# Performance work log

Measured on AMD Instinct MI355X. Metric: run time of the kernel, lower is better.

The kernel has to match this reference:

```python
import math
import jax, jax.numpy as jnp
import numpy as np

B, S, D = 1, 2048, 2048
H, KV, HD = 32, 4, 64  # n_heads, n_kv_heads, head_dim
N_REP = H // KV
ROPE_THETA = 10000.0


def setup_inputs() -> dict:
    key = jax.random.key(0)
    ks = jax.random.split(key, 6)
    x = jax.random.normal(ks[0], (B, S, D), dtype=jnp.float32)
    # precomputed rotary frequencies (real/imag parts of freqs_cis)
    inv_freq = 1.0 / (ROPE_THETA ** (jnp.arange(0, HD, 2, dtype=jnp.float32) / HD))  # [HD/2]
    t = jnp.arange(S, dtype=jnp.float32)
    ang = jnp.outer(t, inv_freq)  # [S, HD/2]
    freqs_cos = jnp.cos(ang)
    freqs_sin = jnp.sin(ang)
    # additive causal mask (large negative instead of -inf; numerically equivalent)
    mask = jnp.where(jnp.tril(jnp.ones((S, S), dtype=bool)), 0.0, -1e9).astype(jnp.float32)
    scale = 0.02
    wq = jax.random.normal(ks[1], (D, H * HD), dtype=jnp.float32) * scale
    wk = jax.random.normal(ks[2], (D, KV * HD), dtype=jnp.float32) * scale
    wv = jax.random.normal(ks[3], (D, KV * HD), dtype=jnp.float32) * scale
    wo = jax.random.normal(ks[4], (H * HD, D), dtype=jnp.float32) * scale
    return {"x": x, "freqs_cos": freqs_cos, "freqs_sin": freqs_sin, "mask": mask,
            "wq": wq, "wk": wk, "wv": wv, "wo": wo}


def _rope(t, cos, sin):
    # t: [B,S,h,HD]; cos/sin: [S, HD/2] -> complex multiply on (even, odd) pairs
    tr = t.reshape(*t.shape[:-1], HD // 2, 2)
    t0, t1 = tr[..., 0], tr[..., 1]
    c = cos[None, :, None, :]
    s = sin[None, :, None, :]
    o0 = t0 * c - t1 * s
    o1 = t0 * s + t1 * c
    return jnp.stack([o0, o1], axis=-1).reshape(t.shape)


def reference(x, freqs_cos, freqs_sin, mask, wq, wk, wv, wo):
    bsz, seqlen, _ = x.shape
    xq = (x @ wq).reshape(bsz, seqlen, H, HD)
    xk = (x @ wk).reshape(bsz, seqlen, KV, HD)
    xv = (x @ wv).reshape(bsz, seqlen, KV, HD)
    xq = _rope(xq, freqs_cos, freqs_sin)
    xk = _rope(xk, freqs_cos, freqs_sin)
    # GQA: repeat kv heads
    xk = jnp.repeat(xk, N_REP, axis=2)  # [B,S,H,HD]
    xv = jnp.repeat(xv, N_REP, axis=2)
    scores = jnp.einsum('bqhd,bkhd->bhqk', xq, xk) / math.sqrt(HD)
    scores = scores + mask[None, None, :, :]
    probs = jax.nn.softmax(scores.astype(jnp.float32), axis=-1).astype(xq.dtype)
    out = jnp.einsum('bhqk,bkhd->bqhd', probs, xv).reshape(bsz, seqlen, H * HD)
    return out @ wo
```

## Files before the change

kernel.cpp:

```cpp
#include <hip/hip_runtime.h>

typedef unsigned short u16;
typedef __attribute__((ext_vector_type(4))) float f32x4;
typedef __attribute__((ext_vector_type(16))) float f32x16;
typedef __attribute__((ext_vector_type(8))) short bf16x8;
typedef __attribute__((ext_vector_type(4))) unsigned short u16x4;
typedef __attribute__((ext_vector_type(4))) unsigned u32x4;
typedef __attribute__((ext_vector_type(2))) unsigned uv2;

__device__ __forceinline__ u16 f2bf(float f) {
  unsigned u = __float_as_uint(f);
  u += 0x7FFFu + ((u >> 16) & 1u);
  return (u16)(u >> 16);
}
__device__ __forceinline__ float bf2f(u16 v) {
  return __uint_as_float(((unsigned)v) << 16);
}

__device__ __forceinline__ void gload_lds16(const u16* g, u16* l) {
  __builtin_amdgcn_global_load_lds((const __attribute__((address_space(1))) void*)g,
                                   (__attribute__((address_space(3))) void*)l, 16, 0, 0);
}

__device__ __forceinline__ unsigned cvt_pk_bf16(float lo, float hi) {
  unsigned r;
  asm("v_cvt_pk_bf16_f32 %0, %1, %2" : "=v"(r) : "v"(lo), "v"(hi));
  return r;
}

__device__ __forceinline__ float fexp2(float x) {
#if __has_builtin(__builtin_amdgcn_exp2f)
  return __builtin_amdgcn_exp2f(x);
#else
  return __expf(x * 0.6931471805599453f);
#endif
}

__global__ __launch_bounds__(256) void convert_f32_bf16(const float* __restrict__ in,
                                                        u16* __restrict__ out, int n) {
  int i = (blockIdx.x * 256 + threadIdx.x) * 4;
  if (i >= n) return;
  float4 v = *(const float4*)&in[i];
  out[i + 0] = f2bf(v.x);
  out[i + 1] = f2bf(v.y);
  out[i + 2] = f2bf(v.z);
  out[i + 3] = f2bf(v.w);
}

__global__ __launch_bounds__(256) void transpose_f32_bf16(const float* __restrict__ in,
                                                          u16* __restrict__ out,
                                                          int R, int C) {
  __shared__ float tile[32][33];
  int c0 = blockIdx.x * 32, r0 = blockIdx.y * 32;
  int tx = threadIdx.x, ty = threadIdx.y;
  for (int j = 0; j < 32; j += 8)
    tile[ty + j][tx] = in[(size_t)(r0 + ty + j) * C + c0 + tx];
  __syncthreads();
  for (int j = 0; j < 32; j += 8)
    out[(size_t)(c0 + ty + j) * R + r0 + tx] = f2bf(tile[tx][ty + j]);
}

__global__ __launch_bounds__(256) void transpose_bf16(const u16* __restrict__ in, int ld_in,
                                                      u16* __restrict__ out, int R, int C) {
  __shared__ u16 tile[32][33];
  int c0 = blockIdx.x * 32, r0 = blockIdx.y * 32;
  int tx = threadIdx.x, ty = threadIdx.y;
  for (int j = 0; j < 32; j += 8)
    tile[ty + j][tx] = in[(size_t)(r0 + ty + j) * ld_in + c0 + tx];
  __syncthreads();
  for (int j = 0; j < 32; j += 8)
    out[(size_t)(c0 + ty + j) * R + r0 + tx] = tile[tx][ty + j];
}

template <bool F32OUT>
__global__ __launch_bounds__(256) void gemm_bt(const u16* __restrict__ A,
                                               const u16* __restrict__ BT,
                                               void* __restrict__ Cout,
                                               int M, int N, int K) {
  const int bn = blockIdx.x * 128, bm = blockIdx.y * 128;
  const int tid = threadIdx.x;
  const int wid = tid >> 6, lane = tid & 63;
  const int wr = wid >> 1, wc = wid & 1;
  const int lrow = lane & 15, g = lane >> 4;

  __shared__ __align__(16) u16 As[2][128 * 64];
  __shared__ __align__(16) u16 Bs[2][128 * 64];

  const int srow = tid >> 3;
  const int cswz = (((tid & 7) ^ (srow & 7)) << 3);
  const u16* a_src = A + (size_t)(bm + srow) * K + cswz;
  const u16* b_src = BT + (size_t)(bn + srow) * K + cswz;

  const int rsw = (lrow & 7) << 4;
  const int colsw0 = ((g * 16) ^ rsw) >> 1;
  const int colsw1 = ((64 + g * 16) ^ rsw) >> 1;

#define STAGE(buf, k0)                                                        \
  do {                                                                        \
    const u16* ap = a_src + (k0);                                             \
    const u16* bp = b_src + (k0);                                             \
    u16* ad = &As[buf][0] + tid * 8;                                          \
    u16* bd = &Bs[buf][0] + tid * 8;                                          \
    _Pragma("unroll") for (int p = 0; p < 4; ++p) {                           \
      gload_lds16(ap + (size_t)p * 32 * K, ad + p * 2048);                    \
      gload_lds16(bp + (size_t)p * 32 * K, bd + p * 2048);                    \
    }                                                                         \
  } while (0)

  f32x4 acc[4][4] = {};

  const int nt = K >> 6;
  STAGE(0, 0);
  int cur = 0;
  for (int t = 0; t < nt; ++t) {
    if (t + 1 < nt) {
      STAGE(cur ^ 1, (t + 1) * 64);
      asm volatile("s_waitcnt vmcnt(8)" ::: "memory");
    } else {
      asm volatile("s_waitcnt vmcnt(0)" ::: "memory");
    }
    __builtin_amdgcn_s_barrier();
    asm volatile("" ::: "memory");

    bf16x8 af[4][2], bfr[4][2];
#pragma unroll
    for (int m = 0; m < 4; ++m) {
      int row = wr * 64 + m * 16 + lrow;
      af[m][0] = *(const bf16x8*)&As[cur][row * 64 + colsw0];
      af[m][1] = *(const bf16x8*)&As[cur][row * 64 + colsw1];
    }
#pragma unroll
    for (int n = 0; n < 4; ++n) {
      int row = wc * 64 + n * 16 + lrow;
      bfr[n][0] = *(const bf16x8*)&Bs[cur][row * 64 + colsw0];
      bfr[n][1] = *(const bf16x8*)&Bs[cur][row * 64 + colsw1];
    }
#pragma unroll
    for (int ks = 0; ks < 2; ++ks)
#pragma unroll
      for (int m = 0; m < 4; ++m)
#pragma unroll
        for (int n = 0; n < 4; ++n)
          acc[m][n] =
              __builtin_amdgcn_mfma_f32_16x16x32_bf16(af[m][ks], bfr[n][ks], acc[m][n], 0, 0, 0);

    asm volatile("" ::: "memory");
    __builtin_amdgcn_s_barrier();
    cur ^= 1;
  }
#undef STAGE

#pragma unroll
  for (int m = 0; m < 4; ++m) {
    int row0 = bm + wr * 64 + m * 16 + (g << 2);
#pragma unroll
    for (int n = 0; n < 4; ++n) {
      int col = bn + wc * 64 + n * 16 + lrow;
#pragma unroll
      for (int r = 0; r < 4; ++r) {
        if constexpr (F32OUT)
          ((float*)Cout)[(size_t)(row0 + r) * N + col] = acc[m][n][r];
        else
          ((u16*)Cout)[(size_t)(row0 + r) * N + col] = f2bf(acc[m][n][r]);
      }
    }
  }
}

__global__ __launch_bounds__(256) void rope_kernel(u16* __restrict__ QKV,
                                                   const float* __restrict__ cosT,
                                                   const float* __restrict__ sinT) {
  int idx = blockIdx.x * 256 + threadIdx.x;
  if (idx >= 2048 * 1152) return;
  int row = idx / 1152, p = idx - row * 1152;
  int col = p * 2;
  size_t off = (size_t)row * 2560 + col;
  float t0 = bf2f(QKV[off]), t1 = bf2f(QKV[off + 1]);
  int i = (col & 63) >> 1;
  float c = cosT[row * 32 + i], s = sinT[row * 32 + i];
  QKV[off] = f2bf(t0 * c - t1 * s);
  QKV[off + 1] = f2bf(t0 * s + t1 * c);
}

__global__ __launch_bounds__(512) void attn_kernel(const u16* __restrict__ QKV,
                                                   const u16* __restrict__ VT,
                                                   u16* __restrict__ attn_out) {
  const int h = blockIdx.x;
  const int qb = (int)gridDim.y - 1 - (int)blockIdx.y;
  const int tid = threadIdx.x, w = tid >> 6, lane = tid & 63;
  const int wq4 = w & 3, half = w >> 2;
  const int l31 = lane & 31, hh = lane >> 5;
  const int kh = h >> 3;
  const int q0w = qb * 128 + wq4 * 32;
  const int qg = q0w + l31;

  __shared__ __align__(16) u16 smem[32768];

  const int srow8 = lane >> 3;
  const int scol = (((lane & 7) ^ srow8) << 3);

#define ASTAGE(buf, kb)                                                              \
  do {                                                                               \
    u16* kd = smem + (half * 2 + (buf)) * 4096 + (wq4 * 8) * 64 + lane * 8;          \
    u16* vd = smem + 16384 + (half * 2 + (buf)) * 4096 + (wq4 * 8) * 64 + lane * 8;  \
    _Pragma("unroll") for (int p = 0; p < 2; ++p) {                                  \
      int rr = p * 32 + wq4 * 8 + srow8;                                             \
      gload_lds16(QKV + (size_t)((kb) + rr) * 2560 + 2048 + kh * 64 + scol,          \
                  kd + p * 2048);                                                    \
      gload_lds16(VT + (size_t)(kh * 64 + rr) * 2048 + (kb) + scol, vd + p * 2048);  \
    }                                                                                \
  } while (0)

  bf16x8 qf[4];
  {
    size_t base = (size_t)qg * 2560 + h * 64 + hh * 8;
#pragma unroll
    for (int ks = 0; ks < 4; ++ks) qf[ks] = *(const bf16x8*)&QKV[base + ks * 16];
  }

  const int ksw = (l31 & 7) << 3;

  f32x16 acc0 = {}, acc1 = {};
  float mrun = -1e30f, lrun = 0.f;
  const float SC = 0.125f * 1.44269504088896f;

  const int NT = qb + 1;
  ASTAGE(0, half * 64);
  int cur = 0;

  for (int t = 0; t < NT; ++t) {
    const int kb = (2 * t + half) * 64;
    if (t + 1 < NT) {
      ASTAGE(cur ^ 1, kb + 128);
      asm volatile("s_waitcnt vmcnt(4)" ::: "memory");
    } else {
      asm volatile("s_waitcnt vmcnt(0)" ::: "memory");
    }
    __builtin_amdgcn_s_barrier();
    asm volatile("" ::: "memory");

    if (kb <= q0w + 31) {
      const u16* Kc = smem + (half * 2 + cur) * 4096;
      const u16* Vc = smem + 16384 + (half * 2 + cur) * 4096;

      f32x16 sc0 = {}, sc1 = {};
      __builtin_amdgcn_s_setprio(1);
#pragma unroll
      for (int ks = 0; ks < 4; ++ks) {
        int c = (ks * 16 + hh * 8) ^ ksw;
        bf16x8 kf0 = *(const bf16x8*)&Kc[l31 * 64 + c];
        bf16x8 kf1 = *(const bf16x8*)&Kc[(32 + l31) * 64 + c];
        sc0 = __builtin_amdgcn_mfma_f32_32x32x16_bf16(kf0, qf[ks], sc0, 0, 0, 0);
        sc1 = __builtin_amdgcn_mfma_f32_32x32x16_bf16(kf1, qf[ks], sc1, 0, 0, 0);
      }
      __builtin_amdgcn_s_setprio(0);

      if (kb + 63 > q0w) {
#pragma unroll
        for (int r = 0; r < 16; ++r) {
          int keyoff = (r & 3) + 8 * (r >> 2) + 4 * hh;
          if (kb + keyoff > qg) sc0[r] = -1e5f;
          if (kb + 32 + keyoff > qg) sc1[r] = -1e5f;
        }
      }

      float m8[8];
#pragma unroll
      for (int i = 0; i < 8; ++i)
        m8[i] = fmaxf(fmaxf(sc0[i], sc0[i + 8]), fmaxf(sc1[i], sc1[i + 8]));
#pragma unroll
      for (int st = 4; st >= 1; st >>= 1)
#pragma unroll
        for (int i = 0; i < st; ++i) m8[i] = fmaxf(m8[i], m8[i + st]);
      float mx = fmaxf(m8[0], __shfl_xor(m8[0], 32, 64));
      float mxs = mx * SC;

      if (__any(mxs > mrun + 8.f)) {
        float nm = fmaxf(mrun, mxs);
        float fs = fexp2(mrun - nm);
        mrun = nm;
        lrun *= fs;
#pragma unroll
        for (int i = 0; i < 16; ++i) { acc0[i] *= fs; acc1[i] *= fs; }
      }

      float p0[16], p1[16];
      const float nmn = -mrun;
#pragma unroll
      for (int i = 0; i < 16; ++i) {
        p0[i] = fexp2(__builtin_fmaf(sc0[i], SC, nmn));
        p1[i] = fexp2(__builtin_fmaf(sc1[i], SC, nmn));
      }
      float s8[8];
#pragma unroll
      for (int i = 0; i < 8; ++i) s8[i] = (p0[i] + p0[i + 8]) + (p1[i] + p1[i + 8]);
#pragma unroll
      for (int st = 4; st >= 1; st >>= 1)
#pragma unroll
        for (int i = 0; i < st; ++i) s8[i] += s8[i + st];
      lrun += s8[0] + __shfl_xor(s8[0], 32, 64);

      bf16x8 pf[4];
#pragma unroll
      for (int tt = 0; tt < 2; ++tt) {
        const float* pp = tt ? p1 : p0;
        unsigned wd[8];
#pragma unroll
        for (int j = 0; j < 8; ++j) wd[j] = cvt_pk_bf16(pp[2 * j], pp[2 * j + 1]);
        uv2 sA = __builtin_amdgcn_permlane32_swap(wd[0], wd[2], false, false);
        uv2 sB = __builtin_amdgcn_permlane32_swap(wd[1], wd[3], false, false);
        uv2 sC = __builtin_amdgcn_permlane32_swap(wd[4], wd[6], false, false);
        uv2 sD = __builtin_amdgcn_permlane32_swap(wd[5], wd[7], false, false);
        u32x4 f0 = {sA[0], sB[0], sA[1], sB[1]};
        u32x4 f1 = {sC[0], sD[0], sC[1], sD[1]};
        pf[tt * 2 + 0] = __builtin_bit_cast(bf16x8, f0);
        pf[tt * 2 + 1] = __builtin_bit_cast(bf16x8, f1);
      }

      __builtin_amdgcn_s_setprio(1);
#pragma unroll
      for (int ks = 0; ks < 4; ++ks) {
        int c = (ks * 16 + hh * 8) ^ ksw;
        bf16x8 vf0 = *(const bf16x8*)&Vc[l31 * 64 + c];
        bf16x8 vf1 = *(const bf16x8*)&Vc[(32 + l31) * 64 + c];
        acc0 = __builtin_amdgcn_mfma_f32_32x32x16_bf16(vf0, pf[ks], acc0, 0, 0, 0);
        acc1 = __builtin_amdgcn_mfma_f32_32x32x16_bf16(vf1, pf[ks], acc1, 0, 0, 0);
      }
      __builtin_amdgcn_s_setprio(0);
    }

    asm volatile("" ::: "memory");
    __builtin_amdgcn_s_barrier();
    cur ^= 1;
  }
#undef ASTAGE

  float* MRG = (float*)smem;
  float4* CH = (float4*)smem;
  if (half == 1) {
#pragma unroll
    for (int c = 0; c < 4; ++c) {
      float4 v0 = {acc0[4 * c + 0], acc0[4 * c + 1], acc0[4 * c + 2], acc0[4 * c + 3]};
      float4 v1 = {acc1[4 * c + 0], acc1[4 * c + 1], acc1[4 * c + 2], acc1[4 * c + 3]};
      CH[(wq4 * 8 + c) * 64 + lane] = v0;
      CH[(wq4 * 8 + 4 + c) * 64 + lane] = v1;
    }
    MRG[8192 + wq4 * 128 + lane * 2 + 0] = mrun;
    MRG[8192 + wq4 * 128 + lane * 2 + 1] = lrun;
  }
  __syncthreads();
  if (half == 0) {
    float m1 = MRG[8192 + wq4 * 128 + lane * 2 + 0];
    float l1 = MRG[8192 + wq4 * 128 + lane * 2 + 1];
    float m = fmaxf(mrun, m1);
    float f0 = fexp2(mrun - m), f1 = fexp2(m1 - m);
    float inv = 1.f / (lrun * f0 + l1 * f1);
    float a = f0 * inv, b = f1 * inv;
    size_t obase = (size_t)qg * 2048 + h * 64;
#pragma unroll
    for (int c = 0; c < 4; ++c) {
      float4 r0 = CH[(wq4 * 8 + c) * 64 + lane];
      float4 r1 = CH[(wq4 * 8 + 4 + c) * 64 + lane];
      u16x4 o0, o1;
      o0[0] = f2bf(acc0[4 * c + 0] * a + r0.x * b);
      o0[1] = f2bf(acc0[4 * c + 1] * a + r0.y * b);
      o0[2] = f2bf(acc0[4 * c + 2] * a + r0.z * b);
      o0[3] = f2bf(acc0[4 * c + 3] * a + r0.w * b);
      o1[0] = f2bf(acc1[4 * c + 0] * a + r1.x * b);
      o1[1] = f2bf(acc1[4 * c + 1] * a + r1.y * b);
      o1[2] = f2bf(acc1[4 * c + 2] * a + r1.z * b);
      o1[3] = f2bf(acc1[4 * c + 3] * a + r1.w * b);
      *(u16x4*)&attn_out[obase + 8 * c + 4 * hh] = o0;
      *(u16x4*)&attn_out[obase + 32 + 8 * c + 4 * hh] = o1;
    }
  }
}

extern "C" void kernel_launch(void* const* d_in, const int* in_sizes, int n_in,
                              void* d_out, int out_size, void* d_ws, size_t ws_size,
                              hipStream_t stream) {
  const float* x = (const float*)d_in[0];
  const float* fcos = (const float*)d_in[1];
  const float* fsin = (const float*)d_in[2];
  const float* wq = (const float*)d_in[4];
  const float* wk = (const float*)d_in[5];
  const float* wv = (const float*)d_in[6];
  const float* wo = (const float*)d_in[7];

  char* ws = (char*)d_ws;
  u16* xb    = (u16*)(ws);
  u16* wqkvT = (u16*)(ws + (8u << 20));
  u16* woT   = (u16*)(ws + (18u << 20));
  u16* QKV   = (u16*)(ws + (26u << 20));
  u16* VT    = (u16*)(ws + (36u << 20));
  u16* attn  = xb;

  dim3 tb32(32, 8);

  convert_f32_bf16<<<4096, 256, 0, stream>>>(x, xb, 2048 * 2048);
  transpose_f32_bf16<<<dim3(64, 64), tb32, 0, stream>>>(wq, wqkvT, 2048, 2048);
  transpose_f32_bf16<<<dim3(8, 64), tb32, 0, stream>>>(wk, wqkvT + (size_t)2048 * 2048, 2048, 256);
  transpose_f32_bf16<<<dim3(8, 64), tb32, 0, stream>>>(wv, wqkvT + (size_t)2304 * 2048, 2048, 256);
  transpose_f32_bf16<<<dim3(64, 64), tb32, 0, stream>>>(wo, woT, 2048, 2048);

  gemm_bt<false><<<dim3(20, 16), 256, 0, stream>>>(xb, wqkvT, QKV, 2048, 2560, 2048);

  rope_kernel<<<9216, 256, 0, stream>>>(QKV, fcos, fsin);

  transpose_bf16<<<dim3(8, 64), tb32, 0, stream>>>(QKV + 2304, 2560, VT, 2048, 256);

  attn_kernel<<<dim3(32, 16), 512, 0, stream>>>(QKV, VT, attn);

  gemm_bt<true><<<dim3(16, 16), 256, 0, stream>>>(attn, woT, d_out, 2048, 2048, 2048);
}
```

Baseline: 139.8 us.

## Fuse RoPE into QKV GEMM epilogue, merge weight transposes, use 8-wave GEMM

Applies the rotary embedding inside the QKV GEMM epilogue, using a lane shuffle to fetch the paired element, and removes the separate rope kernel and its extra read-modify-write pass over QKV. The three Q/K/V weight transposes are merged into a single launch. The GEMM now runs with 512 threads (8 waves, 2x4 layout), each wave computing a 64x32 sub-tile, and the staging, swizzle and waitcnt values are adjusted to match. This raises the number of waves available to hide latency, at the cost of more LDS fragment loads per MFMA and a slightly more expensive epilogue.

```diff
diff --git a/kernel.cpp b/kernel.cpp
--- a/kernel.cpp
+++ b/kernel.cpp
@@ -60,6 +60,25 @@
     out[(size_t)(c0 + ty + j) * R + r0 + tx] = f2bf(tile[tx][ty + j]);
 }
 
+__global__ __launch_bounds__(256) void transpose_wqkv(const float* __restrict__ wq,
+                                                      const float* __restrict__ wk,
+                                                      const float* __restrict__ wv,
+                                                      u16* __restrict__ out) {
+  __shared__ float tile[32][33];
+  int bx = blockIdx.x, r0 = blockIdx.y * 32;
+  const float* src;
+  int C, cc0;
+  if (bx < 64) { src = wq; C = 2048; cc0 = bx * 32; }
+  else if (bx < 72) { src = wk; C = 256; cc0 = (bx - 64) * 32; }
+  else { src = wv; C = 256; cc0 = (bx - 72) * 32; }
+  int tx = threadIdx.x, ty = threadIdx.y;
+  for (int j = 0; j < 32; j += 8)
+    tile[ty + j][tx] = src[(size_t)(r0 + ty + j) * C + cc0 + tx];
+  __syncthreads();
+  for (int j = 0; j < 32; j += 8)
+    out[(size_t)(bx * 32 + ty + j) * 2048 + r0 + tx] = f2bf(tile[tx][ty + j]);
+}
+
 __global__ __launch_bounds__(256) void transpose_bf16(const u16* __restrict__ in, int ld_in,
                                                       u16* __restrict__ out, int R, int C) {
   __shared__ u16 tile[32][33];
@@ -72,15 +91,17 @@
     out[(size_t)(c0 + ty + j) * R + r0 + tx] = tile[tx][ty + j];
 }
 
-template <bool F32OUT>
-__global__ __launch_bounds__(256) void gemm_bt(const u16* __restrict__ A,
-                                               const u16* __restrict__ BT,
-                                               void* __restrict__ Cout,
-                                               int M, int N, int K) {
+template <bool F32OUT, bool DO_ROPE>
+__global__ __launch_bounds__(512, 4) void gemm_bt(const u16* __restrict__ A,
+                                                  const u16* __restrict__ BT,
+                                                  void* __restrict__ Cout,
+                                                  int M, int N, int K,
+                                                  const float* __restrict__ cosT,
+                                                  const float* __restrict__ sinT) {
   const int bn = blockIdx.x * 128, bm = blockIdx.y * 128;
   const int tid = threadIdx.x;
   const int wid = tid >> 6, lane = tid & 63;
-  const int wr = wid >> 1, wc = wid & 1;
+  const int wr = wid >> 2, wc = wid & 3;
   const int lrow = lane & 15, g = lane >> 4;
 
   __shared__ __align__(16) u16 As[2][128 * 64];
@@ -91,9 +112,9 @@
   const u16* a_src = A + (size_t)(bm + srow) * K + cswz;
   const u16* b_src = BT + (size_t)(bn + srow) * K + cswz;
 
-  const int rsw = (lrow & 7) << 4;
-  const int colsw0 = ((g * 16) ^ rsw) >> 1;
-  const int colsw1 = ((64 + g * 16) ^ rsw) >> 1;
+  const int swz16 = (lrow & 7) << 3;
+  const int colsw0 = (g * 8) ^ swz16;
+  const int colsw1 = (32 + g * 8) ^ swz16;
 
 #define STAGE(buf, k0)                                                        \
   do {                                                                        \
@@ -101,13 +122,13 @@
     const u16* bp = b_src + (k0);                                             \
     u16* ad = &As[buf][0] + tid * 8;                                          \
     u16* bd = &Bs[buf][0] + tid * 8;                                          \
-    _Pragma("unroll") for (int p = 0; p < 4; ++p) {                           \
-      gload_lds16(ap + (size_t)p * 32 * K, ad + p * 2048);                    \
-      gload_lds16(bp + (size_t)p * 32 * K, bd + p * 2048);                    \
+    _Pragma("unroll") for (int p = 0; p < 2; ++p) {                           \
+      gload_lds16(ap + (size_t)p * 64 * K, ad + p * 4096);                    \
+      gload_lds16(bp + (size_t)p * 64 * K, bd + p * 4096);                    \
     }                                                                         \
   } while (0)
 
-  f32x4 acc[4][4] = {};
+  f32x4 acc[4][2] = {};
 
   const int nt = K >> 6;
   STAGE(0, 0);
@@ -115,14 +136,14 @@
   for (int t = 0; t < nt; ++t) {
     if (t + 1 < nt) {
       STAGE(cur ^ 1, (t + 1) * 64);
-      asm volatile("s_waitcnt vmcnt(8)" ::: "memory");
+      asm volatile("s_waitcnt vmcnt(4)" ::: "memory");
     } else {
       asm volatile("s_waitcnt vmcnt(0)" ::: "memory");
     }
     __builtin_amdgcn_s_barrier();
     asm volatile("" ::: "memory");
 
-    bf16x8 af[4][2], bfr[4][2];
+    bf16x8 af[4][2], bfr[2][2];
 #pragma unroll
     for (int m = 0; m < 4; ++m) {
       int row = wr * 64 + m * 16 + lrow;
@@ -130,8 +151,8 @@
       af[m][1] = *(const bf16x8*)&As[cur][row * 64 + colsw1];
     }
 #pragma unroll
-    for (int n = 0; n < 4; ++n) {
-      int row = wc * 64 + n * 16 + lrow;
+    for (int n = 0; n < 2; ++n) {
+      int row = wc * 32 + n * 16 + lrow;
       bfr[n][0] = *(const bf16x8*)&Bs[cur][row * 64 + colsw0];
       bfr[n][1] = *(const bf16x8*)&Bs[cur][row * 64 + colsw1];
     }
@@ -140,7 +161,7 @@
 #pragma unroll
       for (int m = 0; m < 4; ++m)
 #pragma unroll
-        for (int n = 0; n < 4; ++n)
+        for (int n = 0; n < 2; ++n)
           acc[m][n] =
               __builtin_amdgcn_mfma_f32_16x16x32_bf16(af[m][ks], bfr[n][ks], acc[m][n], 0, 0, 0);
 
@@ -154,32 +175,31 @@
   for (int m = 0; m < 4; ++m) {
     int row0 = bm + wr * 64 + m * 16 + (g << 2);
 #pragma unroll
-    for (int n = 0; n < 4; ++n) {
-      int col = bn + wc * 64 + n * 16 + lrow;
+    for (int n = 0; n < 2; ++n) {
+      int col = bn + wc * 32 + n * 16 + lrow;
+      f32x4 v = acc[m][n];
+      if constexpr (DO_ROPE) {
+        if (bn < 2304) {
+          int i = (col & 63) >> 1;
+          float sg = (col & 1) ? 1.f : -1.f;
+#pragma unroll
+          for (int r = 0; r < 4; ++r) {
+            float pv = __shfl_xor(v[r], 1, 64);
+            float c = cosT[(row0 + r) * 32 + i];
+            float s = sinT[(row0 + r) * 32 + i];
+            v[r] = v[r] * c + pv * s * sg;
+          }
+        }
+      }
 #pragma unroll
       for (int r = 0; r < 4; ++r) {
         if constexpr (F32OUT)
-          ((float*)Cout)[(size_t)(row0 + r) * N + col] = acc[m][n][r];
+          ((float*)Cout)[(size_t)(row0 + r) * N + col] = v[r];
         else
-          ((u16*)Cout)[(size_t)(row0 + r) * N + col] = f2bf(acc[m][n][r]);
-      }
-    }
-  }
-}
-
-__global__ __launch_bounds__(256) void rope_kernel(u16* __restrict__ QKV,
-                                                   const float* __restrict__ cosT,
-                                                   const float* __restrict__ sinT) {
-  int idx = blockIdx.x * 256 + threadIdx.x;
-  if (idx >= 2048 * 1152) return;
-  int row = idx / 1152, p = idx - row * 1152;
-  int col = p * 2;
-  size_t off = (size_t)row * 2560 + col;
-  float t0 = bf2f(QKV[off]), t1 = bf2f(QKV[off + 1]);
-  int i = (col & 63) >> 1;
-  float c = cosT[row * 32 + i], s = sinT[row * 32 + i];
-  QKV[off] = f2bf(t0 * c - t1 * s);
-  QKV[off + 1] = f2bf(t0 * s + t1 * c);
+          ((u16*)Cout)[(size_t)(row0 + r) * N + col] = f2bf(v[r]);
+      }
+    }
+  }
 }
 
 __global__ __launch_bounds__(512) void attn_kernel(const u16* __restrict__ QKV,
@@ -398,18 +418,16 @@
   dim3 tb32(32, 8);
 
   convert_f32_bf16<<<4096, 256, 0, stream>>>(x, xb, 2048 * 2048);
-  transpose_f32_bf16<<<dim3(64, 64), tb32, 0, stream>>>(wq, wqkvT, 2048, 2048);
-  transpose_f32_bf16<<<dim3(8, 64), tb32, 0, stream>>>(wk, wqkvT + (size_t)2048 * 2048, 2048, 256);
-  transpose_f32_bf16<<<dim3(8, 64), tb32, 0, stream>>>(wv, wqkvT + (size_t)2304 * 2048, 2048, 256);
+  transpose_wqkv<<<dim3(80, 64), tb32, 0, stream>>>(wq, wk, wv, wqkvT);
   transpose_f32_bf16<<<dim3(64, 64), tb32, 0, stream>>>(wo, woT, 2048, 2048);
 
-  gemm_bt<false><<<dim3(20, 16), 256, 0, stream>>>(xb, wqkvT, QKV, 2048, 2560, 2048);
-
-  rope_kernel<<<9216, 256, 0, stream>>>(QKV, fcos, fsin);
+  gemm_bt<false, true><<<dim3(20, 16), 512, 0, stream>>>(xb, wqkvT, QKV, 2048, 2560, 2048,
+                                                         fcos, fsin);
 
   transpose_bf16<<<dim3(8, 64), tb32, 0, stream>>>(QKV + 2304, 2560, VT, 2048, 256);
 
   attn_kernel<<<dim3(32, 16), 512, 0, stream>>>(QKV, VT, attn);
 
-  gemm_bt<true><<<dim3(16, 16), 256, 0, stream>>>(attn, woT, d_out, 2048, 2048, 2048);
-}
+  gemm_bt<true, false><<<dim3(16, 16), 512, 0, stream>>>(attn, woT, d_out, 2048, 2048, 2048,
+                                                         nullptr, nullptr);
+}
```

Result: faster. 126.7 us (-9.4%).
